# Kernel optimization log

Hardware: AMD Instinct MI355X
Metric: run time of the kernel (lower is better)

The kernel has to match this reference:

```python
import jax, jax.numpy as jnp
import numpy as np

MINING_MARGIN = 0.1
MARGIN = 0.3
EPS = 1e-6  # torch F.pairwise_distance adds eps to the elementwise difference


def _normalize(v):
    # torch F.normalize(p=2): v / max(||v||, 1e-12)
    n = jnp.linalg.norm(v, axis=-1, keepdims=True)
    return v / jnp.maximum(n, 1e-12)


def setup_inputs() -> dict:
    key = jax.random.key(0)
    x = jax.random.normal(key, (16384, 2, 256), dtype=jnp.float32)
    return {"x": x}


def reference(x):
    a = _normalize(x[:, 0, :])  # [B, D] anchors
    p = _normalize(x[:, 1, :])  # [B, D] positives
    # mining uses detached embeddings
    ad = jax.lax.stop_gradient(a)
    pd = jax.lax.stop_gradient(p)
    B, d = ad.shape

    # Full pairwise distance matrix D[i, j] = ||ad[i] - pd[j] + EPS||_2,
    # expanded algebraically to avoid a [B, B, D] intermediate:
    # ||a - p + e||^2 = ||a||^2 + ||p||^2 - 2 a.p + 2e*(sum(a) - sum(p)) + d*e^2
    dot = ad @ pd.T                                   # [B, B]
    na2 = jnp.sum(ad * ad, axis=1)                    # [B]
    np2 = jnp.sum(pd * pd, axis=1)                    # [B]
    sa = jnp.sum(ad, axis=1)                          # [B]
    sp = jnp.sum(pd, axis=1)                          # [B]
    D2 = (na2[:, None] + np2[None, :] - 2.0 * dot
          + 2.0 * EPS * (sa[:, None] - sp[None, :]) + d * EPS * EPS)
    D = jnp.sqrt(jnp.clip(D2, 0.0))                   # [B, B]

    diag = jnp.diagonal(D)                            # anchor-to-own-positive dist
    # semihard: farther than positive but within mining_margin
    mask = (D > diag[:, None]) & (D < diag[:, None] + MINING_MARGIN)

    # GPU-side uniform random choice per row among masked candidates
    k1, k2 = jax.random.split(jax.random.key(1))
    g = jax.random.uniform(k1, (B, B))
    scores = jnp.where(mask, g, -1.0)
    cand = jnp.argmax(scores, axis=1)                 # random masked index
    fallback = jax.random.randint(k2, (B,), 0, B)     # random.choice(posidx)
    negidx = jnp.where(jnp.any(mask, axis=1), cand, fallback)

    neg = p[negidx]                                   # [B, D]
    pos_dist = jnp.linalg.norm(a - p + EPS, axis=1)
    neg_dist = jnp.linalg.norm(a - neg + EPS, axis=1)
    loss = jnp.mean(jax.nn.relu(pos_dist ** 2 - neg_dist ** 2 + MARGIN))
    return loss
```

## Files before the change

### kernel.cpp

```cpp
#include <hip/hip_runtime.h>
#include <stdint.h>

#define B_N 16384
#define DIMV 256
#define XSTRIDE 512
#define EPSF 1e-6f
#define CEF 2.56e-10f
#define TWOEPS 2e-6f
#define MINING 0.1f
#define MARGINF 0.3f
#define NSTRIP 8

typedef __attribute__((ext_vector_type(8))) short bf16x8;
typedef __attribute__((ext_vector_type(4))) float f32x4;

__device__ __forceinline__ void tf2x32(uint32_t k0, uint32_t k1,
                                       uint32_t& x0, uint32_t& x1) {
  uint32_t k2 = k0 ^ k1 ^ 0x1BD11BDAu;
  x0 += k0; x1 += k1;
#define TFR(r) { x0 += x1; x1 = (x1 << (r)) | (x1 >> (32 - (r))); x1 ^= x0; }
  TFR(13) TFR(15) TFR(26) TFR(6)
  x0 += k1; x1 += k2 + 1u;
  TFR(17) TFR(29) TFR(16) TFR(24)
  x0 += k2; x1 += k0 + 2u;
  TFR(13) TFR(15) TFR(26) TFR(6)
  x0 += k0; x1 += k1 + 3u;
  TFR(17) TFR(29) TFR(16) TFR(24)
  x0 += k1; x1 += k2 + 4u;
  TFR(13) TFR(15) TFR(26) TFR(6)
  x0 += k2; x1 += k0 + 5u;
#undef TFR
}

#define TF_ROT(x, r) __builtin_amdgcn_alignbit((x), (x), 32u - (r))

__device__ __forceinline__ uint32_t tf_mb(uint32_t K0, uint32_t K1, uint32_t c1) {
  const uint32_t K2 = K0 ^ K1 ^ 0x1BD11BDAu;
  uint32_t x0 = K0;
  uint32_t x1 = c1 + K1;
#define R4A { x0 += x1; x1 = TF_ROT(x1, 13); x1 ^= x0; \
              x0 += x1; x1 = TF_ROT(x1, 15); x1 ^= x0; \
              x0 += x1; x1 = TF_ROT(x1, 26); x1 ^= x0; \
              x0 += x1; x1 = TF_ROT(x1, 6);  x1 ^= x0; }
#define R4B { x0 += x1; x1 = TF_ROT(x1, 17); x1 ^= x0; \
              x0 += x1; x1 = TF_ROT(x1, 29); x1 ^= x0; \
              x0 += x1; x1 = TF_ROT(x1, 16); x1 ^= x0; \
              x0 += x1; x1 = TF_ROT(x1, 24); x1 ^= x0; }
  R4A; x0 += K1; x1 += K2 + 1u;
  R4B; x0 += K2; x1 += K0 + 2u;
  R4A; x0 += K0; x1 += K1 + 3u;
  R4B; x0 += K1; x1 += K2 + 4u;
  R4A; x0 += K2; x1 += K0 + 5u;
#undef R4A
#undef R4B
  return (x0 ^ x1) >> 9;
}

__device__ __forceinline__ float wave_sum(float v) {
#pragma unroll
  for (int off = 32; off > 0; off >>= 1) v += __shfl_xor(v, off, 64);
  return v;
}

__device__ __forceinline__ void gl_lds16(const unsigned short* g, unsigned short* s) {
  __builtin_amdgcn_global_load_lds(
      (const __attribute__((address_space(1))) void*)g,
      (__attribute__((address_space(3))) void*)s, 16, 0, 0);
}

__device__ __forceinline__ uint32_t split_pack(float v) {
  const uint32_t u = __float_as_uint(v);
  const uint32_t hi = (u + 0x7FFFu + ((u >> 16) & 1u)) >> 16;
  const float hf = __uint_as_float(hi << 16);
  const float lf = v - hf;
  const uint32_t ul = __float_as_uint(lf);
  const uint32_t lo = (ul + 0x7FFFu + ((ul >> 16) & 1u)) >> 16;
  return hi | (lo << 16);
}

__global__ void k1_stats(const float* __restrict__ x, float* __restrict__ invA,
                         float* __restrict__ invP, float* __restrict__ rowA,
                         float* __restrict__ colB, float* __restrict__ lo,
                         float* __restrict__ pos2) {
  const int i = blockIdx.x;
  const int l = threadIdx.x;
  const float4 va = *(const float4*)&x[i * XSTRIDE + l * 4];
  const float4 vp = *(const float4*)&x[i * XSTRIDE + DIMV + l * 4];
  float saa = va.x*va.x + va.y*va.y + va.z*va.z + va.w*va.w;
  float spp = vp.x*vp.x + vp.y*vp.y + vp.z*vp.z + vp.w*vp.w;
  saa = wave_sum(saa); spp = wave_sum(spp);
  const float ia = 1.0f / fmaxf(sqrtf(saa), 1e-12f);
  const float ip = 1.0f / fmaxf(sqrtf(spp), 1e-12f);
  const float ax = va.x*ia, ay = va.y*ia, az = va.z*ia, aw = va.w*ia;
  const float px = vp.x*ip, py = vp.y*ip, pz = vp.z*ip, pw = vp.w*ip;
  float na2 = ax*ax + ay*ay + az*az + aw*aw;
  float np2 = px*px + py*py + pz*pz + pw*pw;
  float sa  = ax + ay + az + aw;
  float sp  = px + py + pz + pw;
  float dii = ax*px + ay*py + az*pz + aw*pw;
  const float dx = ax-px+EPSF, dy = ay-py+EPSF, dz = az-pz+EPSF, dw = aw-pw+EPSF;
  float ps = dx*dx + dy*dy + dz*dz + dw*dw;
  na2 = wave_sum(na2); np2 = wave_sum(np2); sa = wave_sum(sa);
  sp  = wave_sum(sp);  dii = wave_sum(dii); ps = wave_sum(ps);
  if (l == 0) {
    const float rA = na2 + TWOEPS * sa + CEF;
    const float cB = np2 - TWOEPS * sp;
    invA[i] = ia; invP[i] = ip; rowA[i] = rA; colB[i] = cB;
    lo[i] = sqrtf(fmaxf(rA + cB - 2.0f * dii, 0.0f));
    pos2[i] = ps;
  }
}

__global__ void k1b_cvt(const float* __restrict__ x, const float* __restrict__ invA,
                        const float* __restrict__ invP,
                        unsigned short* __restrict__ Abf,
                        unsigned short* __restrict__ Pbf) {
  const int t = blockIdx.x * 256 + threadIdx.x;
  const int row = t >> 6, l = t & 63;
  const float ia = invA[row], ip = invP[row];
  const float4 va = *(const float4*)&x[row * XSTRIDE + l * 4];
  const float4 vp = *(const float4*)&x[row * XSTRIDE + DIMV + l * 4];
  uint4 oa, op;
  oa.x = split_pack(va.x * ia); oa.y = split_pack(va.y * ia);
  oa.z = split_pack(va.z * ia); oa.w = split_pack(va.w * ia);
  op.x = split_pack(vp.x * ip); op.y = split_pack(vp.y * ip);
  op.z = split_pack(vp.z * ip); op.w = split_pack(vp.w * ip);
  *(uint4*)&Abf[(size_t)row * 512 + l * 8] = oa;
  *(uint4*)&Pbf[(size_t)row * 512 + l * 8] = op;
}

__global__ __launch_bounds__(256, 2) void k2_mfma(
    const unsigned short* __restrict__ Abf, const unsigned short* __restrict__ Pbf,
    const float* __restrict__ rowA, const float* __restrict__ colB,
    const float* __restrict__ lo, unsigned long long* __restrict__ partials) {
  __shared__ __align__(16) unsigned short As[128 * 64];
  __shared__ __align__(16) unsigned short Bs[128 * 64];
  __shared__ unsigned long long red[128][2];

  const int tid = threadIdx.x;
  const int w = tid >> 6;
  const int l = tid & 63;
  const int q = l >> 4;
  const int c16 = l & 15;
  const int rBase = blockIdx.x * 128;
  const int strip = blockIdx.y;
  const int wR = (w >> 1) * 64;
  const int wC = (w & 1) * 64;

  uint32_t K0 = 0u, K1 = 0u;
  tf2x32(0u, 1u, K0, K1);

  const int sw = c16 & 7;
  const int sgk = (l & 7) ^ ((l >> 3) & 7);

  const int arow = rBase + w * 32 + (l >> 3);
  const unsigned short* gA0 = Abf + (size_t)arow * 512 + sgk * 8;
  unsigned short* lA0 = &As[(w * 32) * 64];
  unsigned short* lB0 = &Bs[(w * 32) * 64];

  float Lr[16], Hr[16];
  const int iBase = rBase + wR + q * 4;
#pragma unroll
  for (int ri = 0; ri < 16; ++ri) {
    const int i = iBase + (ri >> 2) * 16 + (ri & 3);
    const float ra = rowA[i];
    const float lv = lo[i];
    Lr[ri] = lv * lv - ra;
    Hr[ri] = (lv + MINING) * (lv + MINING) - ra;
  }

  int bmb[16], bj[16];
#pragma unroll
  for (int ri = 0; ri < 16; ++ri) { bmb[ri] = -1; bj[ri] = 0; }

  for (int ct = 0; ct < 16; ++ct) {
    const int cBase = strip * 2048 + ct * 128;
    const int brow = cBase + w * 32 + (l >> 3);
    const unsigned short* gB0 = Pbf + (size_t)brow * 512 + sgk * 8;

    f32x4 acc[4][4];
#pragma unroll
    for (int m = 0; m < 4; ++m)
#pragma unroll
      for (int n = 0; n < 4; ++n) {
        f32x4 z = {0.0f, 0.0f, 0.0f, 0.0f};
        acc[m][n] = z;
      }

    for (int kc = 0; kc < 512; kc += 64) {
      __syncthreads();
#pragma unroll
      for (int u = 0; u < 4; ++u) {
        gl_lds16(gA0 + kc + u * 8 * 512, lA0 + u * 8 * 64);
        gl_lds16(gB0 + kc + u * 8 * 512, lB0 + u * 8 * 64);
      }
      __syncthreads();
#pragma unroll
      for (int ks = 0; ks < 2; ++ks) {
        const int px = ((ks * 4 + q) ^ sw) * 8;
        bf16x8 am[4], bn[4];
#pragma unroll
        for (int m = 0; m < 4; ++m)
          am[m] = *(const bf16x8*)&As[(wR + m * 16 + c16) * 64 + px];
#pragma unroll
        for (int n = 0; n < 4; ++n)
          bn[n] = *(const bf16x8*)&Bs[(wC + n * 16 + c16) * 64 + px];
#pragma unroll
        for (int m = 0; m < 4; ++m)
#pragma unroll
          for (int n = 0; n < 4; ++n)
            acc[m][n] = __builtin_amdgcn_mfma_f32_16x16x32_bf16(
                am[m], bn[n], acc[m][n], 0, 0, 0);
      }
    }

    int jc[4]; float colBc[4];
#pragma unroll
    for (int n = 0; n < 4; ++n) {
      jc[n] = cBase + wC + n * 16 + c16;
      colBc[n] = colB[jc[n]];
    }
#pragma unroll
    for (int ri = 0; ri < 16; ++ri) {
      const int m = ri >> 2, r = ri & 3;
      const int i = iBase + m * 16 + r;
      const uint32_t ihi = ((uint32_t)i) << 14;
      const float Lv = Lr[ri], Hv = Hr[ri];
      int b = bmb[ri], j0 = bj[ri];
#pragma unroll
      for (int n = 0; n < 4; ++n) {
        const float t = fmaf(-2.0f, acc[m][n][r], colBc[n]);
        const uint32_t mb = tf_mb(K0, K1, ihi | (uint32_t)jc[n]);
        const bool upd = (t > Lv) & (t < Hv) & (jc[n] != i) & ((int)mb > b);
        b  = upd ? (int)mb : b;
        j0 = upd ? jc[n] : j0;
      }
      bmb[ri] = b; bj[ri] = j0;
    }
  }

#pragma unroll
  for (int ri = 0; ri < 16; ++ri) {
    unsigned long long bk = 0ull;
    if (bmb[ri] >= 0)
      bk = ((unsigned long long)(uint32_t)(bmb[ri] + 1) << 32) |
           (unsigned long long)(uint32_t)(16383 - bj[ri]);
#pragma unroll
    for (int off = 1; off < 16; off <<= 1) {
      const unsigned long long o = __shfl_xor(bk, off, 64);
      if (o > bk) bk = o;
    }
    if (c16 == 0) red[wR + (ri >> 2) * 16 + q * 4 + (ri & 3)][w & 1] = bk;
  }
  __syncthreads();
  if (tid < 128) {
    const unsigned long long g0 = red[tid][0], g1 = red[tid][1];
    partials[(size_t)(rBase + tid) * NSTRIP + strip] = g0 > g1 ? g0 : g1;
  }
}

#define TM 64
#define TN 128
#define KC 64
#define AS_LD 68
#define BS_LD 132
#define COLS_PER_STRIP (B_N / NSTRIP)
#define TILES_PER_STRIP (COLS_PER_STRIP / TN)

__global__ __launch_bounds__(256, 3) void k2_mine(
    const float* __restrict__ x, const float* __restrict__ invA,
    const float* __restrict__ invP, const float* __restrict__ rowA,
    const float* __restrict__ colB, const float* __restrict__ lo,
    unsigned long long* __restrict__ partials) {
  __shared__ __align__(16) float As[KC * AS_LD];
  __shared__ __align__(16) float Bs[KC * BS_LD];
  __shared__ float colBs[TN];

  const int tid = threadIdx.x;
  const int ty = tid >> 4;
  const int tx = tid & 15;
  const int rBase = blockIdx.x * TM;
  const int strip = blockIdx.y;
  const int cStart = strip * COLS_PER_STRIP;

  uint32_t k1h = 0u, k1l = 0u;
  tf2x32(0u, 1u, k1h, k1l);

  float rowA_r[4], lo_r[4];
  int rows[4];
#pragma unroll
  for (int m = 0; m < 4; ++m) {
    rows[m] = rBase + ty * 4 + m;
    rowA_r[m] = rowA[rows[m]];
    lo_r[m] = lo[rows[m]];
  }

  unsigned long long best[4] = {0ull, 0ull, 0ull, 0ull};
  const int skq = tid & 15;
  const int srr = tid >> 4;

  for (int ct = 0; ct < TILES_PER_STRIP; ++ct) {
    const int cBase = cStart + ct * TN;
    float acc[4][8];
#pragma unroll
    for (int m = 0; m < 4; ++m)
#pragma unroll
      for (int n = 0; n < 8; ++n) acc[m][n] = 0.0f;

    for (int kc = 0; kc < DIMV; kc += KC) {
      __syncthreads();
#pragma unroll
      for (int u = 0; u < 4; ++u) {
        const int r = srr + 16 * u;
        const int row = rBase + r;
        const float4 v = *(const float4*)&x[row * XSTRIDE + kc + skq * 4];
        const float s = invA[row];
        As[(skq * 4 + 0) * AS_LD + r] = v.x * s;
        As[(skq * 4 + 1) * AS_LD + r] = v.y * s;
        As[(skq * 4 + 2) * AS_LD + r] = v.z * s;
        As[(skq * 4 + 3) * AS_LD + r] = v.w * s;
      }
#pragma unroll
      for (int u = 0; u < 8; ++u) {
        const int c = srr + 16 * u;
        const int col = cBase + c;
        const float4 v = *(const float4*)&x[col * XSTRIDE + DIMV + kc + skq * 4];
        const float s = invP[col];
        Bs[(skq * 4 + 0) * BS_LD + c] = v.x * s;
        Bs[(skq * 4 + 1) * BS_LD + c] = v.y * s;
        Bs[(skq * 4 + 2) * BS_LD + c] = v.z * s;
        Bs[(skq * 4 + 3) * BS_LD + c] = v.w * s;
      }
      if (kc == 0 && tid < TN) colBs[tid] = colB[cBase + tid];
      __syncthreads();

#pragma unroll 8
      for (int k = 0; k < KC; ++k) {
        const float4 a4 = *(const float4*)&As[k * AS_LD + ty * 4];
        const float4 bl = *(const float4*)&Bs[k * BS_LD + tx * 4];
        const float4 bh = *(const float4*)&Bs[k * BS_LD + 64 + tx * 4];
        const float am[4] = {a4.x, a4.y, a4.z, a4.w};
        const float bn[8] = {bl.x, bl.y, bl.z, bl.w, bh.x, bh.y, bh.z, bh.w};
#pragma unroll
        for (int m = 0; m < 4; ++m)
#pragma unroll
          for (int n = 0; n < 8; ++n)
            acc[m][n] = fmaf(am[m], bn[n], acc[m][n]);
      }
    }

#pragma unroll
    for (int m = 0; m < 4; ++m) {
      const int i = rows[m];
      const float loi = lo_r[m];
      const float hii = loi + MINING;
#pragma unroll
      for (int n = 0; n < 8; ++n) {
        const int cOff = (n < 4) ? (tx * 4 + n) : (64 + tx * 4 + (n - 4));
        const int j = cBase + cOff;
        const float D2 = rowA_r[m] + colBs[cOff] - 2.0f * acc[m][n];
        const float D = sqrtf(fmaxf(D2, 0.0f));
        if (D > loi && D < hii && j != i) {
          uint32_t c0 = 0u;
          uint32_t c1 = ((uint32_t)i << 14) | (uint32_t)j;
          tf2x32(k1h, k1l, c0, c1);
          const uint32_t bits = c0 ^ c1;
          const uint32_t mb = bits >> 9;
          const unsigned long long pk =
              ((unsigned long long)(mb + 1u) << 32) |
              (unsigned long long)(uint32_t)(16383 - j);
          if (pk > best[m]) best[m] = pk;
        }
      }
    }
  }

  __syncthreads();
  unsigned long long* red = (unsigned long long*)As;
#pragma unroll
  for (int m = 0; m < 4; ++m) red[(ty * 4 + m) * 16 + tx] = best[m];
  __syncthreads();
  if (tid < TM) {
    unsigned long long g = red[tid * 16];
#pragma unroll
    for (int t = 1; t < 16; ++t) {
      const unsigned long long v = red[tid * 16 + t];
      if (v > g) g = v;
    }
    partials[(size_t)(rBase + tid) * NSTRIP + strip] = g;
  }
}

__global__ void k3_select(const unsigned long long* __restrict__ partials,
                          int* __restrict__ negidx) {
  const int i = blockIdx.x * 256 + threadIdx.x;
  unsigned long long g = 0ull;
#pragma unroll
  for (int s = 0; s < NSTRIP; ++s) {
    const unsigned long long v = partials[(size_t)i * NSTRIP + s];
    if (v > g) g = v;
  }
  int ng;
  if (g != 0ull) {
    ng = 16383 - (int)(g & 0xFFFFFFFFull);
  } else {
    uint32_t t0 = 0u, t1 = 1u;
    tf2x32(0u, 1u, t0, t1);
    uint32_t u0 = 0u, u1 = 1u;
    tf2x32(t0, t1, u0, u1);
    uint32_t v0 = 0u, v1 = (uint32_t)i;
    tf2x32(u0, u1, v0, v1);
    ng = (int)((v0 ^ v1) & 16383u);
  }
  negidx[i] = ng;
}

__global__ void k4_loss(const float* __restrict__ x, const float* __restrict__ invA,
                        const float* __restrict__ invP, const float* __restrict__ pos2,
                        const int* __restrict__ negidx, float* __restrict__ bsums) {
  const int w = threadIdx.x >> 6;
  const int l = threadIdx.x & 63;
  const int i = blockIdx.x * 4 + w;
  const float ia = invA[i];
  const int ng = negidx[i];
  const float ip = invP[ng];
  const float4 va = *(const float4*)&x[i * XSTRIDE + l * 4];
  const float4 vn = *(const float4*)&x[ng * XSTRIDE + DIMV + l * 4];
  const float dx = va.x * ia - vn.x * ip + EPSF;
  const float dy = va.y * ia - vn.y * ip + EPSF;
  const float dz = va.z * ia - vn.z * ip + EPSF;
  const float dw = va.w * ia - vn.w * ip + EPSF;
  float s = dx*dx + dy*dy + dz*dz + dw*dw;
  s = wave_sum(s);
  __shared__ float bs[4];
  if (l == 0) bs[w] = fmaxf(pos2[i] - s + MARGINF, 0.0f);
  __syncthreads();
  if (threadIdx.x == 0) bsums[blockIdx.x] = bs[0] + bs[1] + bs[2] + bs[3];
}

__global__ void k5_reduce(const float* __restrict__ bsums, float* __restrict__ out) {
  float s = 0.0f;
  for (int idx = threadIdx.x; idx < (B_N / 4); idx += 256) s += bsums[idx];
  s = wave_sum(s);
  __shared__ float acc4[4];
  if ((threadIdx.x & 63) == 0) acc4[threadIdx.x >> 6] = s;
  __syncthreads();
  if (threadIdx.x == 0)
    out[0] = (acc4[0] + acc4[1] + acc4[2] + acc4[3]) * (1.0f / (float)B_N);
}

extern "C" void kernel_launch(void* const* d_in, const int* in_sizes, int n_in,
                              void* d_out, int out_size, void* d_ws, size_t ws_size,
                              hipStream_t stream) {
  const float* x = (const float*)d_in[0];
  char* ws = (char*)d_ws;
  size_t off = 0;
  unsigned long long* partials = (unsigned long long*)(ws + off);
  off += (size_t)B_N * NSTRIP * sizeof(unsigned long long);
  float* invA = (float*)(ws + off); off += (size_t)B_N * 4;
  float* invP = (float*)(ws + off); off += (size_t)B_N * 4;
  float* rowA = (float*)(ws + off); off += (size_t)B_N * 4;
  float* colB = (float*)(ws + off); off += (size_t)B_N * 4;
  float* lo   = (float*)(ws + off); off += (size_t)B_N * 4;
  float* pos2 = (float*)(ws + off); off += (size_t)B_N * 4;
  int* negidx = (int*)(ws + off);   off += (size_t)B_N * 4;
  float* bsums = (float*)(ws + off); off += (size_t)(B_N / 4) * 4;
  unsigned short* Abf = (unsigned short*)(ws + off);
  off += (size_t)B_N * 512 * sizeof(unsigned short);
  unsigned short* Pbf = (unsigned short*)(ws + off);
  off += (size_t)B_N * 512 * sizeof(unsigned short);
  const size_t ws_need = off;
  float* out = (float*)d_out;

  hipLaunchKernelGGL(k1_stats, dim3(B_N), dim3(64), 0, stream,
                     x, invA, invP, rowA, colB, lo, pos2);
  if (ws_size >= ws_need) {
    hipLaunchKernelGGL(k1b_cvt, dim3(B_N / 4), dim3(256), 0, stream,
                       x, invA, invP, Abf, Pbf);
    hipLaunchKernelGGL(k2_mfma, dim3(B_N / 128, NSTRIP), dim3(256), 0, stream,
                       Abf, Pbf, rowA, colB, lo, partials);
  } else {
    hipLaunchKernelGGL(k2_mine, dim3(B_N / TM, NSTRIP), dim3(256), 0, stream,
                       x, invA, invP, rowA, colB, lo, partials);
  }
  hipLaunchKernelGGL(k3_select, dim3(B_N / 256), dim3(256), 0, stream,
                     partials, negidx);
  hipLaunchKernelGGL(k4_loss, dim3(B_N / 4), dim3(256), 0, stream,
                     x, invA, invP, pos2, negidx, bsums);
  hipLaunchKernelGGL(k5_reduce, dim3(1), dim3(256), 0, stream, bsums, out);
}
```

Measured before the change: 824.9 us.

## Shrink MFMA mining tile to 64 rows with per-wave full column span

Changes the block tile from 128x128 (2x2 waves, each 64x64) to 64x128, with each wave owning 16 rows across all 128 columns. The LDS cross-wave reduction goes away and each wave writes its partials directly. Per-thread accumulator and register state shrink from 16 to 8 accumulators, and twice as many blocks are launched, which can raise occupancy. In exchange, each A fragment is reused across only 8 MFMAs per k-step instead of 16 per four loads, so LDS reads and global B traffic per FLOP roughly double.

```diff
diff --git a/kernel.cpp b/kernel.cpp
--- a/kernel.cpp
+++ b/kernel.cpp
@@ -133,19 +133,16 @@
     const unsigned short* __restrict__ Abf, const unsigned short* __restrict__ Pbf,
     const float* __restrict__ rowA, const float* __restrict__ colB,
     const float* __restrict__ lo, unsigned long long* __restrict__ partials) {
-  __shared__ __align__(16) unsigned short As[128 * 64];
+  __shared__ __align__(16) unsigned short As[64 * 64];
   __shared__ __align__(16) unsigned short Bs[128 * 64];
-  __shared__ unsigned long long red[128][2];
 
   const int tid = threadIdx.x;
   const int w = tid >> 6;
   const int l = tid & 63;
   const int q = l >> 4;
   const int c16 = l & 15;
-  const int rBase = blockIdx.x * 128;
+  const int rBase = blockIdx.x * 64;
   const int strip = blockIdx.y;
-  const int wR = (w >> 1) * 64;
-  const int wC = (w & 1) * 64;
 
   uint32_t K0 = 0u, K1 = 0u;
   tf2x32(0u, 1u, K0, K1);
@@ -153,94 +150,81 @@
   const int sw = c16 & 7;
   const int sgk = (l & 7) ^ ((l >> 3) & 7);
 
-  const int arow = rBase + w * 32 + (l >> 3);
+  const int arow = rBase + w * 16 + (l >> 3);
   const unsigned short* gA0 = Abf + (size_t)arow * 512 + sgk * 8;
-  unsigned short* lA0 = &As[(w * 32) * 64];
+  unsigned short* lA0 = &As[(w * 16) * 64];
   unsigned short* lB0 = &Bs[(w * 32) * 64];
 
-  float Lr[16], Hr[16];
-  const int iBase = rBase + wR + q * 4;
-#pragma unroll
-  for (int ri = 0; ri < 16; ++ri) {
-    const int i = iBase + (ri >> 2) * 16 + (ri & 3);
+  float Lr[4], Hr[4];
+  const int iBase = rBase + w * 16 + q * 4;
+#pragma unroll
+  for (int ri = 0; ri < 4; ++ri) {
+    const int i = iBase + ri;
     const float ra = rowA[i];
     const float lv = lo[i];
     Lr[ri] = lv * lv - ra;
     Hr[ri] = (lv + MINING) * (lv + MINING) - ra;
   }
 
-  int bmb[16], bj[16];
-#pragma unroll
-  for (int ri = 0; ri < 16; ++ri) { bmb[ri] = -1; bj[ri] = 0; }
+  int bmb[4], bj[4];
+#pragma unroll
+  for (int ri = 0; ri < 4; ++ri) { bmb[ri] = -1; bj[ri] = 0; }
 
   for (int ct = 0; ct < 16; ++ct) {
     const int cBase = strip * 2048 + ct * 128;
     const int brow = cBase + w * 32 + (l >> 3);
     const unsigned short* gB0 = Pbf + (size_t)brow * 512 + sgk * 8;
 
-    f32x4 acc[4][4];
-#pragma unroll
-    for (int m = 0; m < 4; ++m)
-#pragma unroll
-      for (int n = 0; n < 4; ++n) {
-        f32x4 z = {0.0f, 0.0f, 0.0f, 0.0f};
-        acc[m][n] = z;
-      }
+    f32x4 acc[8];
+#pragma unroll
+    for (int n = 0; n < 8; ++n) {
+      f32x4 z = {0.0f, 0.0f, 0.0f, 0.0f};
+      acc[n] = z;
+    }
 
     for (int kc = 0; kc < 512; kc += 64) {
       __syncthreads();
 #pragma unroll
-      for (int u = 0; u < 4; ++u) {
+      for (int u = 0; u < 2; ++u)
         gl_lds16(gA0 + kc + u * 8 * 512, lA0 + u * 8 * 64);
+#pragma unroll
+      for (int u = 0; u < 4; ++u)
         gl_lds16(gB0 + kc + u * 8 * 512, lB0 + u * 8 * 64);
-      }
       __syncthreads();
 #pragma unroll
       for (int ks = 0; ks < 2; ++ks) {
         const int px = ((ks * 4 + q) ^ sw) * 8;
-        bf16x8 am[4], bn[4];
-#pragma unroll
-        for (int m = 0; m < 4; ++m)
-          am[m] = *(const bf16x8*)&As[(wR + m * 16 + c16) * 64 + px];
-#pragma unroll
-        for (int n = 0; n < 4; ++n)
-          bn[n] = *(const bf16x8*)&Bs[(wC + n * 16 + c16) * 64 + px];
-#pragma unroll
-        for (int m = 0; m < 4; ++m)
-#pragma unroll
-          for (int n = 0; n < 4; ++n)
-            acc[m][n] = __builtin_amdgcn_mfma_f32_16x16x32_bf16(
-                am[m], bn[n], acc[m][n], 0, 0, 0);
-      }
-    }
-
-    int jc[4]; float colBc[4];
-#pragma unroll
-    for (int n = 0; n < 4; ++n) {
-      jc[n] = cBase + wC + n * 16 + c16;
-      colBc[n] = colB[jc[n]];
-    }
-#pragma unroll
-    for (int ri = 0; ri < 16; ++ri) {
-      const int m = ri >> 2, r = ri & 3;
-      const int i = iBase + m * 16 + r;
-      const uint32_t ihi = ((uint32_t)i) << 14;
-      const float Lv = Lr[ri], Hv = Hr[ri];
-      int b = bmb[ri], j0 = bj[ri];
-#pragma unroll
-      for (int n = 0; n < 4; ++n) {
-        const float t = fmaf(-2.0f, acc[m][n][r], colBc[n]);
-        const uint32_t mb = tf_mb(K0, K1, ihi | (uint32_t)jc[n]);
-        const bool upd = (t > Lv) & (t < Hv) & (jc[n] != i) & ((int)mb > b);
-        b  = upd ? (int)mb : b;
-        j0 = upd ? jc[n] : j0;
-      }
-      bmb[ri] = b; bj[ri] = j0;
-    }
-  }
-
-#pragma unroll
-  for (int ri = 0; ri < 16; ++ri) {
+        const bf16x8 am = *(const bf16x8*)&As[(w * 16 + c16) * 64 + px];
+        bf16x8 bn[8];
+#pragma unroll
+        for (int n = 0; n < 8; ++n)
+          bn[n] = *(const bf16x8*)&Bs[(n * 16 + c16) * 64 + px];
+#pragma unroll
+        for (int n = 0; n < 8; ++n)
+          acc[n] = __builtin_amdgcn_mfma_f32_16x16x32_bf16(am, bn[n], acc[n],
+                                                           0, 0, 0);
+      }
+    }
+
+#pragma unroll
+    for (int n = 0; n < 8; ++n) {
+      const int j = cBase + n * 16 + c16;
+      const float cb = colB[j];
+#pragma unroll
+      for (int ri = 0; ri < 4; ++ri) {
+        const int i = iBase + ri;
+        const float t = fmaf(-2.0f, acc[n][ri], cb);
+        const uint32_t mb = tf_mb(K0, K1, ((uint32_t)i << 14) | (uint32_t)j);
+        const bool upd = (t > Lr[ri]) & (t < Hr[ri]) & (j != i) &
+                         ((int)mb > bmb[ri]);
+        bmb[ri] = upd ? (int)mb : bmb[ri];
+        bj[ri]  = upd ? j : bj[ri];
+      }
+    }
+  }
+
+#pragma unroll
+  for (int ri = 0; ri < 4; ++ri) {
     unsigned long long bk = 0ull;
     if (bmb[ri] >= 0)
       bk = ((unsigned long long)(uint32_t)(bmb[ri] + 1) << 32) |
@@ -250,12 +234,8 @@
       const unsigned long long o = __shfl_xor(bk, off, 64);
       if (o > bk) bk = o;
     }
-    if (c16 == 0) red[wR + (ri >> 2) * 16 + q * 4 + (ri & 3)][w & 1] = bk;
-  }
-  __syncthreads();
-  if (tid < 128) {
-    const unsigned long long g0 = red[tid][0], g1 = red[tid][1];
-    partials[(size_t)(rBase + tid) * NSTRIP + strip] = g0 > g1 ? g0 : g1;
+    if (c16 == 0)
+      partials[(size_t)(iBase + ri) * NSTRIP + strip] = bk;
   }
 }
 
@@ -477,7 +457,7 @@
   if (ws_size >= ws_need) {
     hipLaunchKernelGGL(k1b_cvt, dim3(B_N / 4), dim3(256), 0, stream,
                        x, invA, invP, Abf, Pbf);
-    hipLaunchKernelGGL(k2_mfma, dim3(B_N / 128, NSTRIP), dim3(256), 0, stream,
+    hipLaunchKernelGGL(k2_mfma, dim3(B_N / 64, NSTRIP), dim3(256), 0, stream,
                        Abf, Pbf, rowA, colB, lo, partials);
   } else {
     hipLaunchKernelGGL(k2_mine, dim3(B_N / TM, NSTRIP), dim3(256), 0, stream,
```

Result: no change. 826.1 us (+0.1%).
